# Kernel optimization log

Measured on AMD Instinct MI355X. Metric: run time of the kernel, lower is better.

Reference implementation:

```python
import jax, jax.numpy as jnp
import numpy as np

N_NODES = 50000
N_EDGES = 800000
N_GRAPHS = 64
HEADS = 8
HID = 16
D = HEADS * HID  # 128
N_CLASSES = 10
NEG_SLOPE = 0.2
N_LAYERS = 5


def setup_inputs() -> dict:
    key = jax.random.key(0)
    ks = jax.random.split(key, 12)
    x = jax.random.normal(ks[0], (N_NODES, D), dtype=jnp.float32)
    edge_index = jax.random.randint(ks[1], (2, N_EDGES), 0, N_NODES, dtype=jnp.int32)
    batch = jnp.sort(jax.random.randint(ks[2], (N_NODES,), 0, N_GRAPHS, dtype=jnp.int32))
    s = 1.0 / np.sqrt(D)
    # all 5 GATv2 layers share the same shapes (in = 8*hidden = 128); stack on axis 0
    Wl = jax.random.normal(ks[3], (N_LAYERS, D, D), dtype=jnp.float32) * s
    bl = jnp.zeros((N_LAYERS, D), dtype=jnp.float32)
    Wr = jax.random.normal(ks[4], (N_LAYERS, D, D), dtype=jnp.float32) * s
    br = jnp.zeros((N_LAYERS, D), dtype=jnp.float32)
    att = jax.random.normal(ks[5], (N_LAYERS, HEADS, HID), dtype=jnp.float32) * (1.0 / np.sqrt(HID))
    bias = jnp.zeros((N_LAYERS, D), dtype=jnp.float32)
    Wout = jax.random.normal(ks[6], (D, N_CLASSES), dtype=jnp.float32) * s
    bout = jnp.zeros((N_CLASSES,), dtype=jnp.float32)
    return {"x": x, "edge_index": edge_index, "batch": batch,
            "Wl": Wl, "bl": bl, "Wr": Wr, "br": br, "att": att, "bias": bias,
            "Wout": Wout, "bout": bout}


def gatv2_layer(x, src, dst, Wl, bl, Wr, br, att, bias):
    # x: [N, D_in]; returns [N, HEADS*HID]
    n = x.shape[0]
    xl = (x @ Wl + bl).reshape(n, HEADS, HID)   # source/message transform
    xr = (x @ Wr + br).reshape(n, HEADS, HID)   # target transform
    # GATv2 attention: att . leaky_relu(xl_j + xr_i) per edge, per head
    e = jax.nn.leaky_relu(xl[src] + xr[dst], NEG_SLOPE)          # [E, H, C]
    logits = jnp.einsum('ehc,hc->eh', e, att)                    # [E, H]
    # segment-softmax over incoming edges of each dst node
    m = jax.ops.segment_max(logits, dst, num_segments=n)         # [N, H]
    p = jnp.exp(logits - m[dst])
    denom = jax.ops.segment_sum(p, dst, num_segments=n)          # [N, H]
    alpha = p / denom[dst]                                       # [E, H]
    msg = xl[src] * alpha[:, :, None]                            # [E, H, C]
    out = jax.ops.segment_sum(msg, dst, num_segments=n)
    return out.reshape(n, HEADS * HID) + bias


def reference(x, edge_index, batch, Wl, bl, Wr, br, att, bias, Wout, bout):
    n = x.shape[0]
    # GATv2Conv(add_self_loops=True): append self loops to the edge list
    loops = jnp.arange(n, dtype=edge_index.dtype)
    src = jnp.concatenate([edge_index[0], loops])
    dst = jnp.concatenate([edge_index[1], loops])
    h = x
    for l in range(N_LAYERS):
        h = gatv2_layer(h, src, dst, Wl[l], bl[l], Wr[l], br[l], att[l], bias[l])
        h = jax.nn.elu(h)
    # global mean pool over graphs
    sums = jax.ops.segment_sum(h, batch, num_segments=N_GRAPHS)       # [G, D]
    counts = jax.ops.segment_sum(jnp.ones((n,), h.dtype), batch, num_segments=N_GRAPHS)
    pooled = sums / jnp.maximum(counts, 1.0)[:, None]
    logits = pooled @ Wout + bout
    return jax.nn.log_softmax(logits, axis=1)
```

## Files before the change

kernel.cpp:

```cpp
#include <hip/hip_runtime.h>
#include <hip/hip_bf16.h>
#include <math.h>

#define DD 128
#define HEADS 8
#define HID 16
#define NEG_SLOPE 0.2f
#define N_LAYERS 5
#define N_GRAPHS 64
#define N_CLASSES 10
#define NBINS 256
#define BIN_CAP 8192

typedef __bf16 bf16x8 __attribute__((ext_vector_type(8)));
typedef float f32x4 __attribute__((ext_vector_type(4)));
typedef float f32x2 __attribute__((ext_vector_type(2)));

__device__ __forceinline__ float bflo(unsigned u) { return __uint_as_float(u << 16); }
__device__ __forceinline__ float bfhi(unsigned u) { return __uint_as_float(u & 0xffff0000u); }
__device__ __forceinline__ float bf1(unsigned short us) { return __uint_as_float(((unsigned)us) << 16); }
__device__ __forceinline__ unsigned short f2bf(float f) {
    unsigned u = __float_as_uint(f);
    u += 0x7fffu + ((u >> 16) & 1u);
    return (unsigned short)(u >> 16);
}
__device__ __forceinline__ unsigned pack2bf(float a, float b) {
    return (unsigned)f2bf(a) | ((unsigned)f2bf(b) << 16);
}
__device__ __forceinline__ f32x2 unpk(unsigned u) {
    f32x2 r; r.x = bflo(u); r.y = bfhi(u); return r;
}

#define WCNT (N_LAYERS * 4 * 16 * 64)


__global__ void k_setup(const float* __restrict__ x, unsigned* __restrict__ xb,
                        const float* __restrict__ Wl, const float* __restrict__ Wr,
                        unsigned short* __restrict__ wB,
                        float* __restrict__ pooled, float* __restrict__ counts, int n2) {
    int id = blockIdx.x * 256 + threadIdx.x;
    if (id < n2) {
        float2 v = *(const float2*)(x + 2 * (size_t)id);
        xb[id] = pack2bf(v.x, v.y);
        return;
    }
    id -= n2;
    if (id < WCNT) {
        int lane = id & 63;
        int ntg  = (id >> 6) & 15;
        int ks   = (id >> 10) & 3;
        int l    = id >> 12;
        int q = lane >> 4, r = lane & 15;
        int n = ntg * 16 + r;
        const float* W = ((n < DD) ? Wl : Wr) + (size_t)l * DD * DD;
        int nn = n & (DD - 1);
        size_t off = (size_t)l * (4 * 16 * 64 * 8) + ((size_t)(ks * 16 + ntg) * 64 + lane) * 8;
        for (int j = 0; j < 8; ++j) {
            int k = ks * 32 + q * 8 + j;
            wB[off + j] = f2bf(W[(size_t)k * DD + nn]);
        }
        return;
    }
    id -= WCNT;
    if (id < N_GRAPHS * DD) { pooled[id] = 0.f; return; }
    id -= N_GRAPHS * DD;
    if (id < N_GRAPHS) counts[id] = 0.f;
}


__global__ __launch_bounds__(256) void k_bin_cnt(const int* __restrict__ ei,
        int* __restrict__ cnt, int n_edges, int n_total, int chunk,
        unsigned long long bin_mul) {
    __shared__ int hist[NBINS];
    int tid = threadIdx.x;
    hist[tid] = 0;
    __syncthreads();
    int beg = blockIdx.x * chunk;
    int end = beg + chunk; if (end > n_total) end = n_total;
    for (int e = beg + tid; e < end; e += 256) {
        int d = (e < n_edges) ? ei[n_edges + e] : (e - n_edges);
        int b = (int)(((unsigned long long)(unsigned)d * bin_mul) >> 32);
        atomicAdd(&hist[b], 1);
    }
    __syncthreads();
    cnt[tid * 256 + blockIdx.x] = hist[tid];
}

__global__ __launch_bounds__(256) void k_bin_scan(int* __restrict__ cnt, int* __restrict__ btot) {
    __shared__ int wsum[4];
    int b = blockIdx.x, t = threadIdx.x, wv = t >> 6, ln = t & 63;
    int v = cnt[b * 256 + t];
    int x = v;
#pragma unroll
    for (int ofs = 1; ofs < 64; ofs <<= 1) {
        int tt = __shfl_up(x, ofs);
        if (ln >= ofs) x += tt;
    }
    if (ln == 63) wsum[wv] = x;
    __syncthreads();
    int off = 0;
    for (int k = 0; k < wv; k++) off += wsum[k];
    int incl = off + x;
    cnt[b * 256 + t] = incl - v;
    if (t == 255) btot[b] = incl;
}

__global__ __launch_bounds__(256) void k_tot_scan(const int* __restrict__ btot,
        int* __restrict__ bin_start, int* __restrict__ row_ptr, int n_nodes) {
    __shared__ int wsum[4];
    int t = threadIdx.x, wv = t >> 6, ln = t & 63;
    int v = btot[t];
    int x = v;
#pragma unroll
    for (int ofs = 1; ofs < 64; ofs <<= 1) {
        int tt = __shfl_up(x, ofs);
        if (ln >= ofs) x += tt;
    }
    if (ln == 63) wsum[wv] = x;
    __syncthreads();
    int off = 0;
    for (int k = 0; k < wv; k++) off += wsum[k];
    int incl = off + x;
    bin_start[t] = incl - v;
    if (t == 255) { bin_start[256] = incl; row_ptr[n_nodes] = incl; }
}

__global__ __launch_bounds__(256) void k_bin_scatter(const int* __restrict__ ei,
        const int* __restrict__ cnt, const int* __restrict__ bin_start,
        unsigned* __restrict__ binned, int n_edges, int n_total, int chunk,
        unsigned long long bin_mul) {
    __shared__ int cur[NBINS];
    int tid = threadIdx.x;
    cur[tid] = bin_start[tid] + cnt[tid * 256 + blockIdx.x];
    __syncthreads();
    int beg = blockIdx.x * chunk;
    int end = beg + chunk; if (end > n_total) end = n_total;
    for (int e = beg + tid; e < end; e += 256) {
        int s, d;
        if (e < n_edges) { s = ei[e]; d = ei[n_edges + e]; }
        else { s = d = e - n_edges; }
        int b = (int)(((unsigned long long)(unsigned)d * bin_mul) >> 32);
        int pos = atomicAdd(&cur[b], 1);
        binned[pos] = (unsigned)s | ((unsigned)d << 16);
    }
}

__global__ __launch_bounds__(256) void k_bin_csr(const unsigned* __restrict__ binned,
        const int* __restrict__ bin_start, int* __restrict__ csr_src,
        int* __restrict__ row_ptr, int n_nodes, unsigned long long bin_mul) {
    __shared__ int sbuf[BIN_CAP];
    __shared__ int ldeg[256];
    __shared__ int wsum[4];
    int b = blockIdx.x, t = threadIdx.x, wv = t >> 6, ln = t & 63;
    int lo = (int)(((((unsigned long long)b) << 32) + bin_mul - 1) / bin_mul);
    int hi = (int)(((((unsigned long long)(b + 1)) << 32) + bin_mul - 1) / bin_mul);
    if (hi > n_nodes) hi = n_nodes;
    int estart = bin_start[b], eend = bin_start[b + 1];
    int ne = eend - estart;
    ldeg[t] = 0;
    __syncthreads();
    for (int k = t; k < ne; k += 256) {
        unsigned v = binned[estart + k];
        atomicAdd(&ldeg[(int)(v >> 16) - lo], 1);
    }
    __syncthreads();
    int vdeg = ldeg[t];
    int x = vdeg;
#pragma unroll
    for (int ofs = 1; ofs < 64; ofs <<= 1) {
        int tt = __shfl_up(x, ofs);
        if (ln >= ofs) x += tt;
    }
    if (ln == 63) wsum[wv] = x;
    __syncthreads();
    int off = 0;
    for (int k = 0; k < wv; k++) off += wsum[k];
    int excl = off + x - vdeg;
    if (lo + t < hi) row_ptr[lo + t] = estart + excl;
    __syncthreads();
    ldeg[t] = excl;
    __syncthreads();
    for (int k = t; k < ne; k += 256) {
        unsigned v = binned[estart + k];
        int pos = atomicAdd(&ldeg[(int)(v >> 16) - lo], 1);
        sbuf[pos] = (int)(v & 0xffffu);
    }
    __syncthreads();
    for (int k = t; k < ne; k += 256)
        csr_src[estart + k] = sbuf[k];
}


__global__ __launch_bounds__(256) void k_gemm_mfma(
    const unsigned short* __restrict__ in, const unsigned short* __restrict__ wB,
    const float* __restrict__ bl, const float* __restrict__ br,
    unsigned short* __restrict__ xl, unsigned short* __restrict__ xr, int n_nodes) {
    int w = threadIdx.x >> 6;
    int lane = threadIdx.x & 63;
    int q = lane >> 4, r = lane & 15;
    int blk = blockIdx.x;

    f32x4 acc[4][4] = {};
#pragma unroll
    for (int ks = 0; ks < 4; ++ks) {
        bf16x8 bh[4];
#pragma unroll
        for (int nt = 0; nt < 4; ++nt) {
            int ntg = w * 4 + nt;
            bh[nt] = *(const bf16x8*)(wB + ((size_t)(ks * 16 + ntg) * 64 + lane) * 8);
        }
        bf16x8 ah[4];
#pragma unroll
        for (int mt = 0; mt < 4; ++mt) {
            int node = blk * 64 + mt * 16 + r;
            if (node >= n_nodes) node = n_nodes - 1;
            ah[mt] = *(const bf16x8*)(in + (size_t)node * DD + ks * 32 + q * 8);
        }
#pragma unroll
        for (int mt = 0; mt < 4; ++mt)
#pragma unroll
            for (int nt = 0; nt < 4; ++nt)
                acc[mt][nt] = __builtin_amdgcn_mfma_f32_16x16x32_bf16(ah[mt], bh[nt], acc[mt][nt], 0, 0, 0);
    }
#pragma unroll
    for (int nt = 0; nt < 4; ++nt) {
        int col = w * 64 + nt * 16 + r;
        float bv = (col < DD) ? bl[col] : br[col - DD];
        unsigned short* dstbase = (col < DD) ? (xl + col) : (xr + (col - DD));
#pragma unroll
        for (int mt = 0; mt < 4; ++mt)
#pragma unroll
            for (int reg = 0; reg < 4; ++reg) {
                int node = blk * 64 + mt * 16 + q * 4 + reg;
                if (node < n_nodes)
                    dstbase[(size_t)node * DD] = f2bf(acc[mt][nt][reg] + bv);
            }
    }
}


__global__ __launch_bounds__(256) void k_node_agg(
    const unsigned short* __restrict__ xl, const unsigned short* __restrict__ xr,
    const int* __restrict__ row_ptr, const int* __restrict__ csr_src,
    const float* __restrict__ att, const float* __restrict__ bias,
    unsigned short* __restrict__ h_out, int n_nodes) {
    int tid = threadIdx.x;
    int grp = tid >> 3;
    int j   = tid & 7;
    int node = blockIdx.x * 32 + grp;
    if (node >= n_nodes) return;
    int beg = row_ptr[node], end = row_ptr[node + 1];

    const unsigned short* xrp = xr + (size_t)node * DD + j * 16;
    uint4 xa = *(const uint4*)xrp;
    uint4 xc = *(const uint4*)(xrp + 8);
    f32x2 q0 = unpk(xa.x), q1 = unpk(xa.y), q2 = unpk(xa.z), q3 = unpk(xa.w);
    f32x2 q4 = unpk(xc.x), q5 = unpk(xc.y), q6 = unpk(xc.z), q7 = unpk(xc.w);
    const float* ap = att + j * 16;
    f32x2 at0 = *(const f32x2*)(ap +  0), at1 = *(const f32x2*)(ap +  2);
    f32x2 at2 = *(const f32x2*)(ap +  4), at3 = *(const f32x2*)(ap +  6);
    f32x2 at4 = *(const f32x2*)(ap +  8), at5 = *(const f32x2*)(ap + 10);
    f32x2 at6 = *(const f32x2*)(ap + 12), at7 = *(const f32x2*)(ap + 14);

    float l = 0.f;
    f32x2 A0 = {0.f,0.f}, A1 = {0.f,0.f}, A2 = {0.f,0.f}, A3 = {0.f,0.f};
    f32x2 A4 = {0.f,0.f}, A5 = {0.f,0.f}, A6 = {0.f,0.f}, A7 = {0.f,0.f};

    uint4 rA0, rA1, rB0, rB1;
    rB0 = rB1 = make_uint4(0u, 0u, 0u, 0u);
    int sN = 0;
    {
        const unsigned short* p = xl + (size_t)csr_src[beg] * DD + j * 16;
        rA0 = *(const uint4*)p; rA1 = *(const uint4*)(p + 8);
    }
    if (beg + 1 < end) {
        const unsigned short* p = xl + (size_t)csr_src[beg + 1] * DD + j * 16;
        rB0 = *(const uint4*)p; rB1 = *(const uint4*)(p + 8);
    }
    if (beg + 2 < end) sN = csr_src[beg + 2];

    for (int t = beg; t < end; ++t) {
        uint4 c0 = rA0, c1 = rA1;
        rA0 = rB0; rA1 = rB1;
        if (t + 2 < end) {
            const unsigned short* p = xl + (size_t)sN * DD + j * 16;
            rB0 = *(const uint4*)p; rB1 = *(const uint4*)(p + 8);
        }
        if (t + 3 < end) sN = csr_src[t + 3];

        f32x2 x0 = unpk(c0.x), x1 = unpk(c0.y), x2 = unpk(c0.z), x3 = unpk(c0.w);
        f32x2 x4 = unpk(c1.x), x5 = unpk(c1.y), x6 = unpk(c1.z), x7 = unpk(c1.w);
        f32x2 v0 = x0 + q0, v1 = x1 + q1, v2 = x2 + q2, v3 = x3 + q3;
        f32x2 v4 = x4 + q4, v5 = x5 + q5, v6 = x6 + q6, v7 = x7 + q7;
        f32x2 m0 = __builtin_elementwise_max(v0, v0 * NEG_SLOPE);
        f32x2 m1 = __builtin_elementwise_max(v1, v1 * NEG_SLOPE);
        f32x2 m2 = __builtin_elementwise_max(v2, v2 * NEG_SLOPE);
        f32x2 m3 = __builtin_elementwise_max(v3, v3 * NEG_SLOPE);
        f32x2 m4 = __builtin_elementwise_max(v4, v4 * NEG_SLOPE);
        f32x2 m5 = __builtin_elementwise_max(v5, v5 * NEG_SLOPE);
        f32x2 m6 = __builtin_elementwise_max(v6, v6 * NEG_SLOPE);
        f32x2 m7 = __builtin_elementwise_max(v7, v7 * NEG_SLOPE);
        f32x2 d = m0 * at0;
        d = m1 * at1 + d; d = m2 * at2 + d; d = m3 * at3 + d;
        d = m4 * at4 + d; d = m5 * at5 + d; d = m6 * at6 + d; d = m7 * at7 + d;
        float lg = d.x + d.y;
        float p = __expf(lg);
        l += p;
        f32x2 p2; p2.x = p; p2.y = p;
        A0 = x0 * p2 + A0; A1 = x1 * p2 + A1; A2 = x2 * p2 + A2; A3 = x3 * p2 + A3;
        A4 = x4 * p2 + A4; A5 = x5 * p2 + A5; A6 = x6 * p2 + A6; A7 = x7 * p2 + A7;
    }

    float rl = 1.f / l;
    const float* bp = bias + j * 16;
    f32x2 b0 = *(const f32x2*)(bp +  0), b1 = *(const f32x2*)(bp +  2);
    f32x2 b2 = *(const f32x2*)(bp +  4), b3 = *(const f32x2*)(bp +  6);
    f32x2 b4 = *(const f32x2*)(bp +  8), b5 = *(const f32x2*)(bp + 10);
    f32x2 b6 = *(const f32x2*)(bp + 12), b7 = *(const f32x2*)(bp + 14);
#define ELU1(z) ((z) > 0.f ? (z) : __expf(z) - 1.f)
    f32x2 rl2; rl2.x = rl; rl2.y = rl;
    f32x2 o0 = A0 * rl2 + b0, o1 = A1 * rl2 + b1, o2 = A2 * rl2 + b2, o3 = A3 * rl2 + b3;
    f32x2 o4 = A4 * rl2 + b4, o5 = A5 * rl2 + b5, o6 = A6 * rl2 + b6, o7 = A7 * rl2 + b7;
    uint4 O1, O2;
    O1.x = pack2bf(ELU1(o0.x), ELU1(o0.y));
    O1.y = pack2bf(ELU1(o1.x), ELU1(o1.y));
    O1.z = pack2bf(ELU1(o2.x), ELU1(o2.y));
    O1.w = pack2bf(ELU1(o3.x), ELU1(o3.y));
    O2.x = pack2bf(ELU1(o4.x), ELU1(o4.y));
    O2.y = pack2bf(ELU1(o5.x), ELU1(o5.y));
    O2.z = pack2bf(ELU1(o6.x), ELU1(o6.y));
    O2.w = pack2bf(ELU1(o7.x), ELU1(o7.y));
    unsigned short* op = h_out + (size_t)node * DD + j * 16;
    *(uint4*)op = O1;
    *(uint4*)(op + 8) = O2;
}


__global__ void k_pool2(const unsigned short* __restrict__ h, const int* __restrict__ batch,
                        float* __restrict__ pooled, float* __restrict__ counts,
                        int n_nodes, int chunk) {
    int c = threadIdx.x;
    int beg = blockIdx.x * chunk;
    if (beg >= n_nodes) return;
    int end = beg + chunk; if (end > n_nodes) end = n_nodes;
    int cur = batch[beg];
    float acc = 0.f; int cnt = 0;
    for (int node = beg; node < end; ++node) {
        int g = batch[node];
        if (g != cur) {
            atomicAdd(&pooled[cur * DD + c], acc);
            if (c == 0) atomicAdd(&counts[cur], (float)cnt);
            acc = 0.f; cnt = 0; cur = g;
        }
        acc += bf1(h[(size_t)node * DD + c]);
        cnt++;
    }
    atomicAdd(&pooled[cur * DD + c], acc);
    if (c == 0) atomicAdd(&counts[cur], (float)cnt);
}

__global__ void k_final(const float* __restrict__ pooled, const float* __restrict__ counts,
                        const float* __restrict__ Wout, const float* __restrict__ bout,
                        float* __restrict__ out) {
    __shared__ float slog[N_GRAPHS * N_CLASSES];
    int t = threadIdx.x;
    int g = t / N_CLASSES, c = t % N_CLASSES;
    float cnt = fmaxf(counts[g], 1.f);
    float acc = bout[c];
    for (int k = 0; k < DD; k++)
        acc += (pooled[g * DD + k] / cnt) * Wout[k * N_CLASSES + c];
    slog[t] = acc;
    __syncthreads();
    float mx = -INFINITY;
    for (int j = 0; j < N_CLASSES; j++) mx = fmaxf(mx, slog[g * N_CLASSES + j]);
    float se = 0.f;
    for (int j = 0; j < N_CLASSES; j++) se += __expf(slog[g * N_CLASSES + j] - mx);
    out[t] = acc - mx - __logf(se);
}

extern "C" void kernel_launch(void* const* d_in, const int* in_sizes, int n_in,
                              void* d_out, int out_size, void* d_ws, size_t ws_size,
                              hipStream_t stream) {
    const float* x     = (const float*)d_in[0];
    const int*   ei    = (const int*)d_in[1];
    const int*   batch = (const int*)d_in[2];
    const float* Wl    = (const float*)d_in[3];
    const float* bl    = (const float*)d_in[4];
    const float* Wr    = (const float*)d_in[5];
    const float* br    = (const float*)d_in[6];
    const float* att   = (const float*)d_in[7];
    const float* bias  = (const float*)d_in[8];
    const float* Wout  = (const float*)d_in[9];
    const float* bout  = (const float*)d_in[10];
    float* out = (float*)d_out;

    int n_nodes = in_sizes[0] / DD;
    int n_edges = in_sizes[1] / 2;
    int n_total = n_edges + n_nodes;
    int ND = n_nodes * DD;

    const int WPL = 4 * 16 * 64 * 8;
    unsigned long long bin_mul = (((unsigned long long)NBINS) << 32) / (unsigned)n_nodes;

    unsigned short* hb  = (unsigned short*)d_ws;
    unsigned short* xb  = hb + (size_t)ND;
    unsigned short* xlb = xb + (size_t)ND;
    unsigned short* xrb = xlb + (size_t)ND;
    unsigned short* wB  = xrb + (size_t)ND;
    int*      cnt       = (int*)(wB + (size_t)N_LAYERS * WPL);
    int*      btot      = cnt + NBINS * 256;
    int*      bin_start = btot + NBINS;
    unsigned* binned    = (unsigned*)(bin_start + NBINS + 1);
    int*      csr_src   = (int*)(binned + n_total);
    int*      row_ptr   = csr_src + n_total;
    float*    pooled    = (float*)(row_ptr + n_nodes + 1);
    float*    counts    = pooled + N_GRAPHS * DD;

    dim3 b256(256);
    int gGemm = (n_nodes + 63) / 64;
    int gAgg  = (n_nodes + 31) / 32;
    int chunk = (n_total + 255) / 256;
    int poolBlocks = 1024;
    int poolChunk = (n_nodes + poolBlocks - 1) / poolBlocks;

    int n2 = ND / 2;
    int setupTotal = n2 + WCNT + N_GRAPHS * DD + N_GRAPHS;
    k_setup<<<(setupTotal + 255) / 256, b256, 0, stream>>>(x, (unsigned*)xb, Wl, Wr, wB,
                                                           pooled, counts, n2);
    k_bin_cnt<<<256, b256, 0, stream>>>(ei, cnt, n_edges, n_total, chunk, bin_mul);
    k_bin_scan<<<NBINS, b256, 0, stream>>>(cnt, btot);
    k_tot_scan<<<1, b256, 0, stream>>>(btot, bin_start, row_ptr, n_nodes);
    k_bin_scatter<<<256, b256, 0, stream>>>(ei, cnt, bin_start, binned, n_edges, n_total,
                                            chunk, bin_mul);
    k_bin_csr<<<NBINS, b256, 0, stream>>>(binned, bin_start, csr_src, row_ptr, n_nodes, bin_mul);

    for (int l = 0; l < N_LAYERS; l++) {
        const float* bl_l   = bl   + (size_t)l * DD;
        const float* br_l   = br   + (size_t)l * DD;
        const float* att_l  = att  + (size_t)l * HEADS * HID;
        const float* bias_l = bias + (size_t)l * DD;
        const unsigned short* in = (l == 0) ? xb : hb;

        k_gemm_mfma<<<gGemm, b256, 0, stream>>>(in, wB + (size_t)l * WPL, bl_l, br_l,
                                                xlb, xrb, n_nodes);
        k_node_agg<<<gAgg, b256, 0, stream>>>(xlb, xrb, row_ptr, csr_src, att_l, bias_l, hb, n_nodes);
    }

    k_pool2<<<poolBlocks, dim3(128), 0, stream>>>(hb, batch, pooled, counts, n_nodes, poolChunk);
    k_final<<<1, dim3(N_GRAPHS * N_CLASSES), 0, stream>>>(pooled, counts, Wout, bout, out);
}
```

Measured before the change: 502.6 us.

## Degree-sort nodes for aggregation and fuse bin counting into setup kernel

Adds a single-block counting sort of nodes by in-degree, producing a permutation that the node aggregation kernel uses. Groups of 8 threads in the same wave then handle nodes with equal degree, which is meant to reduce divergence and load imbalance from uneven edge loops. Separately, it merges the bin-count histogram into the setup kernel to save one launch. The sort runs on a single 1024-thread block over 50k nodes, and the permuted node order scatters reads of xr and writes of h_out, so memory locality gets worse.

```diff
diff --git a/kernel.cpp b/kernel.cpp
--- a/kernel.cpp
+++ b/kernel.cpp
@@ -11,6 +11,7 @@
 #define N_CLASSES 10
 #define NBINS 256
 #define BIN_CAP 8192
+#define DCLS 1024
 
 typedef __bf16 bf16x8 __attribute__((ext_vector_type(8)));
 typedef float f32x4 __attribute__((ext_vector_type(4)));
@@ -34,11 +35,30 @@
 #define WCNT (N_LAYERS * 4 * 16 * 64)
 
 
-__global__ void k_setup(const float* __restrict__ x, unsigned* __restrict__ xb,
-                        const float* __restrict__ Wl, const float* __restrict__ Wr,
-                        unsigned short* __restrict__ wB,
-                        float* __restrict__ pooled, float* __restrict__ counts, int n2) {
-    int id = blockIdx.x * 256 + threadIdx.x;
+__global__ __launch_bounds__(256) void k_setup_cnt(
+        const float* __restrict__ x, unsigned* __restrict__ xb,
+        const float* __restrict__ Wl, const float* __restrict__ Wr,
+        unsigned short* __restrict__ wB, float* __restrict__ pooled,
+        float* __restrict__ counts, const int* __restrict__ ei, int* __restrict__ cnt,
+        int n2, int n_edges, int n_total, int chunk, unsigned long long bin_mul) {
+    int blk = blockIdx.x;
+    if (blk < 256) {
+        __shared__ int hist[NBINS];
+        int tid = threadIdx.x;
+        hist[tid] = 0;
+        __syncthreads();
+        int beg = blk * chunk;
+        int end = beg + chunk; if (end > n_total) end = n_total;
+        for (int e = beg + tid; e < end; e += 256) {
+            int d = (e < n_edges) ? ei[n_edges + e] : (e - n_edges);
+            int b = (int)(((unsigned long long)(unsigned)d * bin_mul) >> 32);
+            atomicAdd(&hist[b], 1);
+        }
+        __syncthreads();
+        cnt[tid * 256 + blk] = hist[tid];
+        return;
+    }
+    int id = (blk - 256) * 256 + threadIdx.x;
     if (id < n2) {
         float2 v = *(const float2*)(x + 2 * (size_t)id);
         xb[id] = pack2bf(v.x, v.y);
@@ -68,24 +88,6 @@
 }
 
 
-__global__ __launch_bounds__(256) void k_bin_cnt(const int* __restrict__ ei,
-        int* __restrict__ cnt, int n_edges, int n_total, int chunk,
-        unsigned long long bin_mul) {
-    __shared__ int hist[NBINS];
-    int tid = threadIdx.x;
-    hist[tid] = 0;
-    __syncthreads();
-    int beg = blockIdx.x * chunk;
-    int end = beg + chunk; if (end > n_total) end = n_total;
-    for (int e = beg + tid; e < end; e += 256) {
-        int d = (e < n_edges) ? ei[n_edges + e] : (e - n_edges);
-        int b = (int)(((unsigned long long)(unsigned)d * bin_mul) >> 32);
-        atomicAdd(&hist[b], 1);
-    }
-    __syncthreads();
-    cnt[tid * 256 + blockIdx.x] = hist[tid];
-}
-
 __global__ __launch_bounds__(256) void k_bin_scan(int* __restrict__ cnt, int* __restrict__ btot) {
     __shared__ int wsum[4];
     int b = blockIdx.x, t = threadIdx.x, wv = t >> 6, ln = t & 63;
@@ -191,6 +193,52 @@
 }
 
 
+__global__ __launch_bounds__(1024) void k_degsort(const int* __restrict__ row_ptr,
+        int* __restrict__ perm, int n_nodes) {
+    __shared__ int hist[DCLS];
+    __shared__ int wsum[16];
+    int t = threadIdx.x, wv = t >> 6, ln = t & 63;
+    hist[t] = 0;
+    __syncthreads();
+    for (int i = t; i < n_nodes; i += 1024) {
+        int deg = row_ptr[i + 1] - row_ptr[i];
+        int c = deg < DCLS ? deg : DCLS - 1;
+        atomicAdd(&hist[c], 1);
+    }
+    __syncthreads();
+    int v = hist[t];
+    int x = v;
+#pragma unroll
+    for (int ofs = 1; ofs < 64; ofs <<= 1) {
+        int tt = __shfl_up(x, ofs);
+        if (ln >= ofs) x += tt;
+    }
+    if (ln == 63) wsum[wv] = x;
+    __syncthreads();
+    if (wv == 0 && ln < 16) {
+        int s = wsum[ln];
+#pragma unroll
+        for (int ofs = 1; ofs < 16; ofs <<= 1) {
+            int tt = __shfl_up(s, ofs);
+            if (ln >= ofs) s += tt;
+        }
+        wsum[ln] = s;
+    }
+    __syncthreads();
+    int waveoff = (wv == 0) ? 0 : wsum[wv - 1];
+    int excl = waveoff + x - v;
+    __syncthreads();
+    hist[t] = excl;
+    __syncthreads();
+    for (int i = t; i < n_nodes; i += 1024) {
+        int deg = row_ptr[i + 1] - row_ptr[i];
+        int c = deg < DCLS ? deg : DCLS - 1;
+        int pos = atomicAdd(&hist[c], 1);
+        perm[pos] = i;
+    }
+}
+
+
 __global__ __launch_bounds__(256) void k_gemm_mfma(
     const unsigned short* __restrict__ in, const unsigned short* __restrict__ wB,
     const float* __restrict__ bl, const float* __restrict__ br,
@@ -242,13 +290,15 @@
 __global__ __launch_bounds__(256) void k_node_agg(
     const unsigned short* __restrict__ xl, const unsigned short* __restrict__ xr,
     const int* __restrict__ row_ptr, const int* __restrict__ csr_src,
+    const int* __restrict__ perm,
     const float* __restrict__ att, const float* __restrict__ bias,
     unsigned short* __restrict__ h_out, int n_nodes) {
     int tid = threadIdx.x;
     int grp = tid >> 3;
     int j   = tid & 7;
-    int node = blockIdx.x * 32 + grp;
-    if (node >= n_nodes) return;
+    int idx = blockIdx.x * 32 + grp;
+    if (idx >= n_nodes) return;
+    int node = perm[idx];
     int beg = row_ptr[node], end = row_ptr[node + 1];
 
     const unsigned short* xrp = xr + (size_t)node * DD + j * 16;
@@ -413,7 +463,8 @@
     unsigned* binned    = (unsigned*)(bin_start + NBINS + 1);
     int*      csr_src   = (int*)(binned + n_total);
     int*      row_ptr   = csr_src + n_total;
-    float*    pooled    = (float*)(row_ptr + n_nodes + 1);
+    int*      perm      = row_ptr + n_nodes + 1;
+    float*    pooled    = (float*)(perm + n_nodes);
     float*    counts    = pooled + N_GRAPHS * DD;
 
     dim3 b256(256);
@@ -425,14 +476,16 @@
 
     int n2 = ND / 2;
     int setupTotal = n2 + WCNT + N_GRAPHS * DD + N_GRAPHS;
-    k_setup<<<(setupTotal + 255) / 256, b256, 0, stream>>>(x, (unsigned*)xb, Wl, Wr, wB,
-                                                           pooled, counts, n2);
-    k_bin_cnt<<<256, b256, 0, stream>>>(ei, cnt, n_edges, n_total, chunk, bin_mul);
+    int gSetup = 256 + (setupTotal + 255) / 256;
+
+    k_setup_cnt<<<gSetup, b256, 0, stream>>>(x, (unsigned*)xb, Wl, Wr, wB, pooled, counts,
+                                             ei, cnt, n2, n_edges, n_total, chunk, bin_mul);
     k_bin_scan<<<NBINS, b256, 0, stream>>>(cnt, btot);
     k_tot_scan<<<1, b256, 0, stream>>>(btot, bin_start, row_ptr, n_nodes);
     k_bin_scatter<<<256, b256, 0, stream>>>(ei, cnt, bin_start, binned, n_edges, n_total,
                                             chunk, bin_mul);
     k_bin_csr<<<NBINS, b256, 0, stream>>>(binned, bin_start, csr_src, row_ptr, n_nodes, bin_mul);
+    k_degsort<<<1, dim3(1024), 0, stream>>>(row_ptr, perm, n_nodes);
 
     for (int l = 0; l < N_LAYERS; l++) {
         const float* bl_l   = bl   + (size_t)l * DD;
@@ -443,7 +496,8 @@
 
         k_gemm_mfma<<<gGemm, b256, 0, stream>>>(in, wB + (size_t)l * WPL, bl_l, br_l,
                                                 xlb, xrb, n_nodes);
-        k_node_agg<<<gAgg, b256, 0, stream>>>(xlb, xrb, row_ptr, csr_src, att_l, bias_l, hb, n_nodes);
+        k_node_agg<<<gAgg, b256, 0, stream>>>(xlb, xrb, row_ptr, csr_src, perm,
+                                              att_l, bias_l, hb, n_nodes);
     }
 
     k_pool2<<<poolBlocks, dim3(128), 0, stream>>>(hb, batch, pooled, counts, n_nodes, poolChunk);
```

Measured after the change: 512.2 us. About the same (+1.9%).
